# Kernel optimization log

Hardware: AMD Instinct MI355X
Metric: run time of the kernel (lower is better)

The kernel has to match this reference:

```python
import jax, jax.numpy as jnp
import numpy as np

N_WORDS = 8192   # total words in batch (flattened ragged loop)
CHAR_LEN = 16    # chars per word (padded/fixed instance)
WORD_VOCAB = 50000
CHAR_VOCAB = 128
WORD_DIM = 300
CHAR_DIM = 64
CHAR_HID = 128   # per-direction LSTM hidden
INPUT_DIM = 512
INFO_DIM = WORD_DIM + 2 * CHAR_HID  # 556


def setup_inputs() -> dict:
    key = jax.random.key(0)
    ks = jax.random.split(key, 16)
    s_ih = 1.0 / np.sqrt(CHAR_DIM)
    s_hh = 1.0 / np.sqrt(CHAR_HID)
    s_out = 1.0 / np.sqrt(INFO_DIM)
    return {
        "word_ids": jax.random.randint(ks[0], (N_WORDS,), 0, WORD_VOCAB),
        "char_ids": jax.random.randint(ks[1], (N_WORDS, CHAR_LEN), 0, CHAR_VOCAB),
        "word_table": jax.random.normal(ks[2], (WORD_VOCAB, WORD_DIM), jnp.float32),
        "char_table": jax.random.normal(ks[3], (CHAR_VOCAB, CHAR_DIM), jnp.float32),
        "Wih_f": jax.random.uniform(ks[4], (4 * CHAR_HID, CHAR_DIM), jnp.float32, -s_ih, s_ih),
        "Whh_f": jax.random.uniform(ks[5], (4 * CHAR_HID, CHAR_HID), jnp.float32, -s_hh, s_hh),
        "bih_f": jax.random.uniform(ks[6], (4 * CHAR_HID,), jnp.float32, -s_hh, s_hh),
        "bhh_f": jax.random.uniform(ks[7], (4 * CHAR_HID,), jnp.float32, -s_hh, s_hh),
        "Wih_b": jax.random.uniform(ks[8], (4 * CHAR_HID, CHAR_DIM), jnp.float32, -s_ih, s_ih),
        "Whh_b": jax.random.uniform(ks[9], (4 * CHAR_HID, CHAR_HID), jnp.float32, -s_hh, s_hh),
        "bih_b": jax.random.uniform(ks[10], (4 * CHAR_HID,), jnp.float32, -s_hh, s_hh),
        "bhh_b": jax.random.uniform(ks[11], (4 * CHAR_HID,), jnp.float32, -s_hh, s_hh),
        "W_out": jax.random.uniform(ks[12], (INPUT_DIM, INFO_DIM), jnp.float32, -s_out, s_out),
        "b_out": jax.random.uniform(ks[13], (INPUT_DIM,), jnp.float32, -s_out, s_out),
    }


def _lstm_dir(x, Wih, Whh, bih, bhh, reverse):
    # x: [L, N, D] -> outputs [L, N, H]; PyTorch gate order i,f,g,o; zero init state.
    L, N, _ = x.shape
    H = Whh.shape[1]
    b = bih + bhh

    def step(carry, xt):
        h, c = carry
        gates = xt @ Wih.T + h @ Whh.T + b  # [N, 4H]
        i, f, g, o = jnp.split(gates, 4, axis=-1)
        c = jax.nn.sigmoid(f) * c + jax.nn.sigmoid(i) * jnp.tanh(g)
        h = jax.nn.sigmoid(o) * jnp.tanh(c)
        return (h, c), h

    init = (jnp.zeros((N, H), x.dtype), jnp.zeros((N, H), x.dtype))
    _, hs = jax.lax.scan(step, init, x, reverse=reverse)
    return hs


def reference(word_ids, char_ids, word_table, char_table,
              Wih_f, Whh_f, bih_f, bhh_f,
              Wih_b, Whh_b, bih_b, bhh_b,
              W_out, b_out):
    w = word_table[word_ids]                     # [N, WORD_DIM]
    ce = char_table[char_ids]                    # [N, L, CHAR_DIM]
    x = jnp.transpose(ce, (1, 0, 2))             # [L, N, CHAR_DIM]
    hf = _lstm_dir(x, Wih_f, Whh_f, bih_f, bhh_f, reverse=False)  # [L, N, H]
    hb = _lstm_dir(x, Wih_b, Whh_b, bih_b, bhh_b, reverse=True)   # [L, N, H]
    # torch.sum over char positions of bidirectional outputs
    char_feat = jnp.sum(jnp.concatenate([hf, hb], axis=-1), axis=0)  # [N, 2H]
    feat = jnp.concatenate([w, char_feat], axis=-1)                  # [N, INFO_DIM]
    return jnp.tanh(feat @ W_out.T + b_out)                          # [N, INPUT_DIM]
```

## Files before the change

kernel.cpp:

```cpp
#include <hip/hip_runtime.h>
#include <hip/hip_bf16.h>

typedef __bf16 bf16x8 __attribute__((ext_vector_type(8)));
typedef float  f32x4  __attribute__((ext_vector_type(4)));
typedef int    i32x4  __attribute__((ext_vector_type(4)));

#define N_WORDS   8192
#define CHAR_LEN  16
#define WORD_DIM  300
#define CHAR_DIM  64
#define HID       128
#define G4        512
#define INFO      556
#define KPAD      576
#define OUTD      512
#define WBL       32
#define WBO       32
#define L2E       1.4426950408889634f

__device__ __forceinline__ float tanh_(float x) {
    return 1.0f - 2.0f * __builtin_amdgcn_rcpf(1.0f + __builtin_amdgcn_exp2f((2.0f * L2E) * x));
}

__global__ void prep_kernel(const float* __restrict__ char_table,
                            const float* __restrict__ Wih_f, const float* __restrict__ bih_f,
                            const float* __restrict__ bhh_f,
                            const float* __restrict__ Wih_b, const float* __restrict__ bih_b,
                            const float* __restrict__ bhh_b,
                            const float* __restrict__ W_out,
                            const float* __restrict__ Whh_f, const float* __restrict__ Whh_b,
                            float* __restrict__ preT,
                            __bf16* __restrict__ Wpad, __bf16* __restrict__ WhhB) {
    __shared__ float x[CHAR_DIM];
    if (blockIdx.x < 256) {
        const int dir = blockIdx.x & 1;
        const int cid = blockIdx.x >> 1;
        const float* Wih = dir ? Wih_b : Wih_f;
        const float* b1  = dir ? bih_b : bih_f;
        const float* b2  = dir ? bhh_b : bhh_f;
        if (threadIdx.x < CHAR_DIM) x[threadIdx.x] = char_table[cid * CHAR_DIM + threadIdx.x];
        __syncthreads();
        for (int g = threadIdx.x; g < G4; g += 256) {
            const f32x4* w4 = (const f32x4*)(Wih + g * CHAR_DIM);
            const f32x4* x4 = (const f32x4*)x;
            float s = b1[g] + b2[g];
            #pragma unroll
            for (int d = 0; d < CHAR_DIM / 4; ++d) {
                f32x4 wv = w4[d], xv = x4[d];
                s += wv[0]*xv[0] + wv[1]*xv[1] + wv[2]*xv[2] + wv[3]*xv[3];
            }
            int tt = g >> 7, j = g & (HID - 1);
            float sc = (tt == 2) ? (-2.0f * L2E) : (-L2E);
            preT[(dir * 128 + cid) * G4 + j * 4 + tt] = s * sc;
        }
    } else {
        int idx = (blockIdx.x - 256) * 256 + threadIdx.x;
        if (idx < OUTD * KPAD) {
            int row = idx / KPAD, col = idx - row * KPAD;
            Wpad[idx] = (col < INFO) ? (__bf16)W_out[row * INFO + col] : (__bf16)0.0f;
        } else {
            int j = idx - OUTD * KPAD;
            if (j < 2 * G4 * HID) {
                const float* src = (j < G4 * HID) ? Whh_f : Whh_b;
                int k = (j < G4 * HID) ? j : j - G4 * HID;
                int gate = (k >> 14) & 3;
                float sc = (gate == 2) ? (-2.0f * L2E) : (-L2E);
                WhhB[j] = (__bf16)(src[k] * sc);
            }
        }
    }
}

__global__ __launch_bounds__(512, 2) void lstm_kernel(
        const int*   __restrict__ char_ids,
        const float* __restrict__ preT,
        const __bf16* __restrict__ WhhB,
        __bf16* __restrict__ char_feat) {
    const int dir = blockIdx.y;
    const int wb  = blockIdx.x * WBL;
    const __bf16* Whh = WhhB + dir * G4 * HID;
    const float* preD = preT + dir * 128 * G4;

    const int tid  = threadIdx.x;
    const int wave = tid >> 6;
    const int lane = tid & 63;
    const int col  = lane & 15;
    const int quad = lane >> 4;
    const int jbase = wave * 16;

    __shared__ __bf16 h_lds[2][WBL][136];
    __shared__ int    cidT[CHAR_LEN][WBL];

    {
        int w = tid >> 4, t = tid & 15;
        cidT[t][w] = char_ids[(wb + w) * CHAR_LEN + t] * (G4 * 4);
    }
    for (int i = tid; i < 2 * WBL * 136; i += 512) ((__bf16*)h_lds)[i] = (__bf16)0.0f;

    bf16x8 Bfrag[4][4];
    #pragma unroll
    for (int tt = 0; tt < 4; ++tt) {
        int row = tt * HID + jbase + col;
        #pragma unroll
        for (int ks = 0; ks < 4; ++ks)
            Bfrag[tt][ks] = *(const bf16x8*)(Whh + row * HID + ks * 32 + quad * 8);
    }

    const char* base_lane = (const char*)(preD + (jbase + col) * 4);

    float c[2][4] = {}, sumh[2][4] = {};

    __syncthreads();

    f32x4 nx[2][4];
    {
        const int tc0 = dir ? (CHAR_LEN - 1) : 0;
        #pragma unroll
        for (int mt = 0; mt < 2; ++mt) {
            i32x4 off = *(const i32x4*)(&cidT[tc0][mt * 16 + quad * 4]);
            #pragma unroll
            for (int r = 0; r < 4; ++r)
                nx[mt][r] = *(const f32x4*)(base_lane + off[r]);
        }
    }

    for (int t = 0; t < CHAR_LEN; ++t) {
        const __bf16 (*hc)[136] = h_lds[t & 1];
        __bf16 (*hn)[136] = h_lds[(t + 1) & 1];

        f32x4 acc[2][4];
        #pragma unroll
        for (int mt = 0; mt < 2; ++mt)
            #pragma unroll
            for (int tt = 0; tt < 4; ++tt)
                acc[mt][tt] = (f32x4){nx[mt][0][tt], nx[mt][1][tt], nx[mt][2][tt], nx[mt][3][tt]};

        __builtin_amdgcn_s_setprio(1);
        {
            bf16x8 A0 = *(const bf16x8*)(&hc[col][quad * 8]);
            bf16x8 A1 = *(const bf16x8*)(&hc[16 + col][quad * 8]);
            #pragma unroll
            for (int tt = 0; tt < 4; ++tt) {
                acc[0][tt] = __builtin_amdgcn_mfma_f32_16x16x32_bf16(A0, Bfrag[tt][0], acc[0][tt], 0, 0, 0);
                acc[1][tt] = __builtin_amdgcn_mfma_f32_16x16x32_bf16(A1, Bfrag[tt][0], acc[1][tt], 0, 0, 0);
            }
        }

        if (t + 1 < CHAR_LEN) {
            const int tc = dir ? (CHAR_LEN - 2 - t) : (t + 1);
            #pragma unroll
            for (int mt = 0; mt < 2; ++mt) {
                i32x4 off = *(const i32x4*)(&cidT[tc][mt * 16 + quad * 4]);
                #pragma unroll
                for (int r = 0; r < 4; ++r)
                    nx[mt][r] = *(const f32x4*)(base_lane + off[r]);
            }
        }

        #pragma unroll
        for (int ks = 1; ks < 4; ++ks) {
            bf16x8 A0 = *(const bf16x8*)(&hc[col][ks * 32 + quad * 8]);
            bf16x8 A1 = *(const bf16x8*)(&hc[16 + col][ks * 32 + quad * 8]);
            #pragma unroll
            for (int tt = 0; tt < 4; ++tt) {
                acc[0][tt] = __builtin_amdgcn_mfma_f32_16x16x32_bf16(A0, Bfrag[tt][ks], acc[0][tt], 0, 0, 0);
                acc[1][tt] = __builtin_amdgcn_mfma_f32_16x16x32_bf16(A1, Bfrag[tt][ks], acc[1][tt], 0, 0, 0);
            }
        }
        __builtin_amdgcn_s_setprio(0);

        #pragma unroll
        for (int mt = 0; mt < 2; ++mt)
            #pragma unroll
            for (int r = 0; r < 4; ++r) {
                float ti = __builtin_amdgcn_exp2f(acc[mt][0][r]);
                float tf = __builtin_amdgcn_exp2f(acc[mt][1][r]);
                float tg = __builtin_amdgcn_exp2f(fminf(acc[mt][2][r], 38.0f));
                float to = __builtin_amdgcn_exp2f(acc[mt][3][r]);
                float sf = __builtin_amdgcn_rcpf(1.0f + tf);
                float ig = (1.0f - tg) * __builtin_amdgcn_rcpf((1.0f + ti) * (1.0f + tg));
                float cv = sf * c[mt][r] + ig;
                c[mt][r] = cv;
                float tc = __builtin_amdgcn_exp2f(cv * (-2.0f * L2E));
                float hv = (1.0f - tc) * __builtin_amdgcn_rcpf((1.0f + to) * (1.0f + tc));
                sumh[mt][r] += hv;
                hn[mt * 16 + quad * 4 + r][jbase + col] = (__bf16)hv;
            }
        __syncthreads();
    }

    #pragma unroll
    for (int mt = 0; mt < 2; ++mt)
        #pragma unroll
        for (int r = 0; r < 4; ++r)
            char_feat[(wb + mt * 16 + quad * 4 + r) * 256 + dir * HID + jbase + col]
                = (__bf16)sumh[mt][r];
}

__global__ __launch_bounds__(1024, 4) void out_kernel(
        const int*   __restrict__ word_ids,
        const float* __restrict__ word_table,
        const __bf16* __restrict__ char_feat,
        const __bf16* __restrict__ Wpad,
        const float* __restrict__ b_out,
        float* __restrict__ out) {
    const int wb  = blockIdx.x * WBO;
    const int tid = threadIdx.x;
    const int wave = tid >> 6, lane = tid & 63, col = lane & 15, quad = lane >> 4;
    const int nbase = wave * 32;

    __shared__ __bf16 feat[WBO][584];
    __shared__ int wid[WBO];
    if (tid < WBO) wid[tid] = word_ids[wb + tid];
    __syncthreads();
    for (int idx = tid; idx < WBO * 75; idx += 1024) {
        int row = idx / 75, ch = idx - row * 75;
        f32x4 v = *(const f32x4*)(word_table + wid[row] * WORD_DIM + ch * 4);
        __bf16* d = &feat[row][ch * 4];
        d[0] = (__bf16)v[0]; d[1] = (__bf16)v[1]; d[2] = (__bf16)v[2]; d[3] = (__bf16)v[3];
    }
    {
        int row = tid >> 5, ch = tid & 31;
        bf16x8 v = *(const bf16x8*)(char_feat + (wb + row) * 256 + ch * 8);
        __bf16* d = &feat[row][WORD_DIM + ch * 8];
        #pragma unroll
        for (int e = 0; e < 8; ++e) d[e] = v[e];
    }
    if (tid < WBO * 28) {
        int row = tid / 28, cc = tid - row * 28;
        feat[row][INFO + cc] = (__bf16)0.0f;
    }
    __syncthreads();

    f32x4 acc[2][2];
    #pragma unroll
    for (int mt = 0; mt < 2; ++mt)
        #pragma unroll
        for (int nt = 0; nt < 2; ++nt) acc[mt][nt] = (f32x4){0.f, 0.f, 0.f, 0.f};

    const __bf16* Wp0 = Wpad + (nbase + col) * KPAD;
    const __bf16* Wp1 = Wpad + (nbase + 16 + col) * KPAD;

    #pragma unroll 2
    for (int kb = 0; kb < KPAD / 32; ++kb) {
        const int ko = kb * 32 + quad * 8;
        bf16x8 B0 = *(const bf16x8*)(Wp0 + ko);
        bf16x8 B1 = *(const bf16x8*)(Wp1 + ko);
        bf16x8 A0 = *(const bf16x8*)(&feat[col][ko]);
        bf16x8 A1 = *(const bf16x8*)(&feat[16 + col][ko]);
        acc[0][0] = __builtin_amdgcn_mfma_f32_16x16x32_bf16(A0, B0, acc[0][0], 0, 0, 0);
        acc[1][0] = __builtin_amdgcn_mfma_f32_16x16x32_bf16(A1, B0, acc[1][0], 0, 0, 0);
        acc[0][1] = __builtin_amdgcn_mfma_f32_16x16x32_bf16(A0, B1, acc[0][1], 0, 0, 0);
        acc[1][1] = __builtin_amdgcn_mfma_f32_16x16x32_bf16(A1, B1, acc[1][1], 0, 0, 0);
    }

    #pragma unroll
    for (int nt = 0; nt < 2; ++nt) {
        int n = nbase + nt * 16 + col;
        float bo = b_out[n];
        #pragma unroll
        for (int mt = 0; mt < 2; ++mt)
            #pragma unroll
            for (int r = 0; r < 4; ++r) {
                int word = wb + mt * 16 + quad * 4 + r;
                out[word * OUTD + n] = tanh_(acc[mt][nt][r] + bo);
            }
    }
}

extern "C" void kernel_launch(void* const* d_in, const int* in_sizes, int n_in,
                              void* d_out, int out_size, void* d_ws, size_t ws_size,
                              hipStream_t stream) {
    const int*   word_ids   = (const int*)d_in[0];
    const int*   char_ids   = (const int*)d_in[1];
    const float* word_table = (const float*)d_in[2];
    const float* char_table = (const float*)d_in[3];
    const float* Wih_f = (const float*)d_in[4];
    const float* Whh_f = (const float*)d_in[5];
    const float* bih_f = (const float*)d_in[6];
    const float* bhh_f = (const float*)d_in[7];
    const float* Wih_b = (const float*)d_in[8];
    const float* Whh_b = (const float*)d_in[9];
    const float* bih_b = (const float*)d_in[10];
    const float* bhh_b = (const float*)d_in[11];
    const float* W_out = (const float*)d_in[12];
    const float* b_out = (const float*)d_in[13];

    char* ws = (char*)d_ws;
    float*  preT      = (float*)ws;
    __bf16* WhhB      = (__bf16*)(ws + 524288);
    __bf16* Wpad      = (__bf16*)(ws + 524288 + 262144);
    __bf16* char_feat = (__bf16*)(ws + 524288 + 262144 + 589824);

    prep_kernel<<<256 + (OUTD * KPAD + 2 * G4 * HID + 255) / 256, 256, 0, stream>>>(
        char_table, Wih_f, bih_f, bhh_f, Wih_b, bih_b, bhh_b,
        W_out, Whh_f, Whh_b, preT, Wpad, WhhB);
    lstm_kernel<<<dim3(N_WORDS / WBL, 2), 512, 0, stream>>>(char_ids, preT, WhhB, char_feat);
    out_kernel<<<N_WORDS / WBO, 1024, 0, stream>>>(word_ids, word_table, char_feat, Wpad, b_out,
                                                   (float*)d_out);
}
```

Measured before the change: 205.0 us.

## Software-pipeline LSTM row groups so MFMA overlaps the other group's gate math

The recurrent LSTM loop now splits each 32-word block into two 16-row groups and staggers them by half a step. One group's MFMA recurrence runs while the other group's gate nonlinearities and h stores execute, hiding the dependent transcendental latency behind matrix work. The first step is peeled so it skips the h=0 MFMA, which also removes the LDS zero-initialisation. In exchange there are twice as many block barriers per time step, plus extra prologue and epilogue code.

```diff
diff --git a/kernel.cpp b/kernel.cpp
--- a/kernel.cpp
+++ b/kernel.cpp
@@ -95,7 +95,6 @@
         int w = tid >> 4, t = tid & 15;
         cidT[t][w] = char_ids[(wb + w) * CHAR_LEN + t] * (G4 * 4);
     }
-    for (int i = tid; i < 2 * WBL * 136; i += 512) ((__bf16*)h_lds)[i] = (__bf16)0.0f;
 
     bf16x8 Bfrag[4][4];
     #pragma unroll
@@ -108,93 +107,79 @@
 
     const char* base_lane = (const char*)(preD + (jbase + col) * 4);
 
-    float c[2][4] = {}, sumh[2][4] = {};
-
-    __syncthreads();
-
-    f32x4 nx[2][4];
-    {
-        const int tc0 = dir ? (CHAR_LEN - 1) : 0;
-        #pragma unroll
-        for (int mt = 0; mt < 2; ++mt) {
-            i32x4 off = *(const i32x4*)(&cidT[tc0][mt * 16 + quad * 4]);
-            #pragma unroll
-            for (int r = 0; r < 4; ++r)
-                nx[mt][r] = *(const f32x4*)(base_lane + off[r]);
-        }
-    }
-
-    for (int t = 0; t < CHAR_LEN; ++t) {
-        const __bf16 (*hc)[136] = h_lds[t & 1];
-        __bf16 (*hn)[136] = h_lds[(t + 1) & 1];
-
-        f32x4 acc[2][4];
-        #pragma unroll
-        for (int mt = 0; mt < 2; ++mt)
+    f32x4 nx0[4], nx1[4], acc0[4], acc1[4];
+    float c0[4] = {}, c1[4] = {}, s0[4] = {}, s1[4] = {};
+
+    auto pref = [&](f32x4* nx, int g, int t) {
+        const int tc = dir ? (CHAR_LEN - 1 - t) : t;
+        i32x4 off = *(const i32x4*)(&cidT[tc][g * 16 + quad * 4]);
+        #pragma unroll
+        for (int r = 0; r < 4; ++r)
+            nx[r] = *(const f32x4*)(base_lane + off[r]);
+    };
+    auto accinit = [&](f32x4* acc, const f32x4* nx) {
+        #pragma unroll
+        for (int tt = 0; tt < 4; ++tt)
+            acc[tt] = (f32x4){nx[0][tt], nx[1][tt], nx[2][tt], nx[3][tt]};
+    };
+    auto mfmag = [&](f32x4* acc, int g, int buf) {
+        const __bf16 (*hc)[136] = h_lds[buf];
+        #pragma unroll
+        for (int ks = 0; ks < 4; ++ks) {
+            bf16x8 A = *(const bf16x8*)(&hc[g * 16 + col][ks * 32 + quad * 8]);
             #pragma unroll
             for (int tt = 0; tt < 4; ++tt)
-                acc[mt][tt] = (f32x4){nx[mt][0][tt], nx[mt][1][tt], nx[mt][2][tt], nx[mt][3][tt]};
-
-        __builtin_amdgcn_s_setprio(1);
-        {
-            bf16x8 A0 = *(const bf16x8*)(&hc[col][quad * 8]);
-            bf16x8 A1 = *(const bf16x8*)(&hc[16 + col][quad * 8]);
-            #pragma unroll
-            for (int tt = 0; tt < 4; ++tt) {
-                acc[0][tt] = __builtin_amdgcn_mfma_f32_16x16x32_bf16(A0, Bfrag[tt][0], acc[0][tt], 0, 0, 0);
-                acc[1][tt] = __builtin_amdgcn_mfma_f32_16x16x32_bf16(A1, Bfrag[tt][0], acc[1][tt], 0, 0, 0);
-            }
-        }
-
-        if (t + 1 < CHAR_LEN) {
-            const int tc = dir ? (CHAR_LEN - 2 - t) : (t + 1);
-            #pragma unroll
-            for (int mt = 0; mt < 2; ++mt) {
-                i32x4 off = *(const i32x4*)(&cidT[tc][mt * 16 + quad * 4]);
-                #pragma unroll
-                for (int r = 0; r < 4; ++r)
-                    nx[mt][r] = *(const f32x4*)(base_lane + off[r]);
-            }
-        }
-
-        #pragma unroll
-        for (int ks = 1; ks < 4; ++ks) {
-            bf16x8 A0 = *(const bf16x8*)(&hc[col][ks * 32 + quad * 8]);
-            bf16x8 A1 = *(const bf16x8*)(&hc[16 + col][ks * 32 + quad * 8]);
-            #pragma unroll
-            for (int tt = 0; tt < 4; ++tt) {
-                acc[0][tt] = __builtin_amdgcn_mfma_f32_16x16x32_bf16(A0, Bfrag[tt][ks], acc[0][tt], 0, 0, 0);
-                acc[1][tt] = __builtin_amdgcn_mfma_f32_16x16x32_bf16(A1, Bfrag[tt][ks], acc[1][tt], 0, 0, 0);
-            }
-        }
-        __builtin_amdgcn_s_setprio(0);
-
-        #pragma unroll
-        for (int mt = 0; mt < 2; ++mt)
-            #pragma unroll
-            for (int r = 0; r < 4; ++r) {
-                float ti = __builtin_amdgcn_exp2f(acc[mt][0][r]);
-                float tf = __builtin_amdgcn_exp2f(acc[mt][1][r]);
-                float tg = __builtin_amdgcn_exp2f(fminf(acc[mt][2][r], 38.0f));
-                float to = __builtin_amdgcn_exp2f(acc[mt][3][r]);
-                float sf = __builtin_amdgcn_rcpf(1.0f + tf);
-                float ig = (1.0f - tg) * __builtin_amdgcn_rcpf((1.0f + ti) * (1.0f + tg));
-                float cv = sf * c[mt][r] + ig;
-                c[mt][r] = cv;
-                float tc = __builtin_amdgcn_exp2f(cv * (-2.0f * L2E));
-                float hv = (1.0f - tc) * __builtin_amdgcn_rcpf((1.0f + to) * (1.0f + tc));
-                sumh[mt][r] += hv;
-                hn[mt * 16 + quad * 4 + r][jbase + col] = (__bf16)hv;
-            }
+                acc[tt] = __builtin_amdgcn_mfma_f32_16x16x32_bf16(A, Bfrag[tt][ks], acc[tt], 0, 0, 0);
+        }
+    };
+    auto gates = [&](f32x4* acc, float* c, float* sh, int g, int buf, bool wr) {
+        __bf16 (*hn)[136] = h_lds[buf];
+        #pragma unroll
+        for (int r = 0; r < 4; ++r) {
+            float ti = __builtin_amdgcn_exp2f(acc[0][r]);
+            float tf = __builtin_amdgcn_exp2f(acc[1][r]);
+            float tg = __builtin_amdgcn_exp2f(fminf(acc[2][r], 38.0f));
+            float to = __builtin_amdgcn_exp2f(acc[3][r]);
+            float sf = __builtin_amdgcn_rcpf(1.0f + tf);
+            float ig = (1.0f - tg) * __builtin_amdgcn_rcpf((1.0f + ti) * (1.0f + tg));
+            float cv = sf * c[r] + ig;
+            c[r] = cv;
+            float tc2 = __builtin_amdgcn_exp2f(cv * (-2.0f * L2E));
+            float hv = (1.0f - tc2) * __builtin_amdgcn_rcpf((1.0f + to) * (1.0f + tc2));
+            sh[r] += hv;
+            if (wr) hn[g * 16 + quad * 4 + r][jbase + col] = (__bf16)hv;
+        }
+    };
+
+    __syncthreads();
+
+    pref(nx0, 0, 0);
+    pref(nx1, 1, 0);
+    accinit(acc0, nx0);
+    pref(nx0, 0, 1);
+    accinit(acc1, nx1);
+    gates(acc0, c0, s0, 0, 0, true);
+    __syncthreads();
+
+    for (int t = 1; t < CHAR_LEN; ++t) {
+        accinit(acc0, nx0);
+        mfmag(acc0, 0, (t - 1) & 1);
+        pref(nx1, 1, t);
+        gates(acc1, c1, s1, 1, (t - 1) & 1, true);
         __syncthreads();
-    }
-
-    #pragma unroll
-    for (int mt = 0; mt < 2; ++mt)
-        #pragma unroll
-        for (int r = 0; r < 4; ++r)
-            char_feat[(wb + mt * 16 + quad * 4 + r) * 256 + dir * HID + jbase + col]
-                = (__bf16)sumh[mt][r];
+        accinit(acc1, nx1);
+        mfmag(acc1, 1, (t - 1) & 1);
+        if (t + 1 < CHAR_LEN) pref(nx0, 0, t + 1);
+        gates(acc0, c0, s0, 0, t & 1, t + 1 < CHAR_LEN);
+        __syncthreads();
+    }
+    gates(acc1, c1, s1, 1, 0, false);
+
+    #pragma unroll
+    for (int r = 0; r < 4; ++r) {
+        char_feat[(wb + quad * 4 + r) * 256 + dir * HID + jbase + col]      = (__bf16)s0[r];
+        char_feat[(wb + 16 + quad * 4 + r) * 256 + dir * HID + jbase + col] = (__bf16)s1[r];
+    }
 }
 
 __global__ __launch_bounds__(1024, 4) void out_kernel(
```

Result: no change. 202.4 us (-1.3%).
